# Optimization experiments

Hardware: AMD Instinct MI355X
Metric: run time of the kernel (lower is better)

The kernel has to match this reference:

```python
import jax, jax.numpy as jnp
import numpy as np

C = 512
EPS = 1e-5


def _layer_norm(x, gamma, beta):
    mu = jnp.mean(x, axis=-1, keepdims=True)
    var = jnp.var(x, axis=-1, keepdims=True)
    return (x - mu) * jax.lax.rsqrt(var + EPS) * gamma + beta


def setup_inputs() -> dict:
    key = jax.random.key(0)
    ks = jax.random.split(key, 12)
    B, L = 8, 2048
    s = 1.0 / np.sqrt(C)
    return {
        "x1": jax.random.normal(ks[0], (B, C, L), dtype=jnp.float32),
        "x2": jax.random.normal(ks[1], (B, C, L), dtype=jnp.float32),
        "w_q": jax.random.normal(ks[2], (C, C), dtype=jnp.float32) * s,
        "b_q": jax.random.normal(ks[3], (C,), dtype=jnp.float32) * s,
        "w_k": jax.random.normal(ks[4], (C, C), dtype=jnp.float32) * s,
        "b_k": jax.random.normal(ks[5], (C,), dtype=jnp.float32) * s,
        "w_v1": jax.random.normal(ks[6], (C, C), dtype=jnp.float32) * s,
        "b_v1": jax.random.normal(ks[7], (C,), dtype=jnp.float32) * s,
        "w_v2": jax.random.normal(ks[8], (C, C), dtype=jnp.float32) * s,
        "b_v2": jax.random.normal(ks[9], (C,), dtype=jnp.float32) * s,
        "ln_gamma": jnp.ones((C,), dtype=jnp.float32),
        "ln_beta": jnp.zeros((C,), dtype=jnp.float32),
    }


def reference(x1, x2, w_q, b_q, w_k, b_k, w_v1, b_v1, w_v2, b_v2, ln_gamma, ln_beta):
    # (B, C, L) -> (B, L, C)
    x1 = jnp.swapaxes(x1, 1, 2)
    x2 = jnp.swapaxes(x2, 1, 2)
    # torch Linear: y = x @ W^T + b
    q = jnp.einsum("blc,dc->bld", x1, w_q) + b_q
    k = jnp.einsum("blc,dc->bld", x2, w_k) + b_k
    v1 = jnp.einsum("blc,dc->bld", x1, w_v1) + b_v1
    v2 = jnp.einsum("blc,dc->bld", x2, w_v2) + b_v2
    # shared attention scores [B, L1, L2]
    attn = jnp.einsum("bqc,bkc->bqk", q, k) / jnp.sqrt(jnp.float32(C))
    attn_k = jax.nn.softmax(attn, axis=-1)          # rows (over L2)
    attn_q = jax.nn.softmax(attn, axis=1)           # cols (over L1)
    vk = jnp.einsum("bqk,bkc->bqc", attn_k, v2)     # [B, L1, C]
    vq = jnp.einsum("bqk,bqc->bkc", attn_q, v1)     # [B, L2, C]
    # cross skip + shared layernorm
    r1 = _layer_norm(vk + x1, ln_gamma, ln_beta)
    r2 = _layer_norm(vq + x2, ln_gamma, ln_beta)
    return (jnp.swapaxes(r1, 1, 2), jnp.swapaxes(r2, 1, 2))
```

## Files before the change

kernel.cpp:

```cpp
#include <hip/hip_runtime.h>

#define L_DIM 2048
#define C_DIM 512
#define B_DIM 8

typedef __attribute__((ext_vector_type(8))) short bf16x8;
typedef __attribute__((ext_vector_type(4))) float f32x4;

constexpr size_t SQ  = (size_t)L_DIM * C_DIM;
constexpr size_t SAT = (size_t)L_DIM * L_DIM;
constexpr size_t MC  = (size_t)B_DIM * L_DIM * C_DIM;
constexpr int BL = B_DIM * L_DIM;

__device__ float g_psr[16][BL];
__device__ float g_psc[16][BL];

__device__ __forceinline__ float bf2f(ushort u) {
  union { float f; unsigned int i; } c; c.i = ((unsigned int)u) << 16; return c.f;
}
__device__ __forceinline__ ushort f2bf(float f) {
  union { float f; unsigned int i; } c; c.f = f;
  unsigned int lsb = (c.i >> 16) & 1u;
  return (ushort)((c.i + 0x7FFFu + lsb) >> 16);
}

__device__ __forceinline__ float wave_red_sum(float v) {
  #pragma unroll
  for (int o = 1; o < 64; o <<= 1) v += __shfl_xor(v, o, 64);
  return v;
}

__device__ __forceinline__ void glds16(const ushort* g, ushort* l) {
  __builtin_amdgcn_global_load_lds(
      (const __attribute__((address_space(1))) void*)g,
      (__attribute__((address_space(3))) void*)l, 16, 0, 0);
}

__device__ __forceinline__ int slotAB(int r, int c) {
  return (((c ^ (r & 7)) + (r >> 3)) & 7);
}
__device__ __forceinline__ int chAB(int r, int sl) {
  return ((sl - (r >> 3)) & 7) ^ (r & 7);
}
__device__ __forceinline__ int slotC(int r, int q4) {
  return ((q4 ^ (r & 15)) + (r >> 4)) & 15;
}

__device__ __forceinline__ int xcd_swz(int bid, int nwg) {
  return (bid & 7) * (nwg >> 3) + (bid >> 3);
}

template <bool STATS, bool SCALE>
__device__ __forceinline__ void gemm_core128(
    const ushort* __restrict__ Ab, const ushort* __restrict__ Bb,
    const float* __restrict__ bias,
    ushort* __restrict__ obN, ushort* __restrict__ obT,
    const int K, const int lda, const int ldb, const int ldo, const int ldoT,
    const int m0, const int n0, const float scale, const int EPI,
    const int sb, const float* __restrict__ ps)
{
  __shared__ __align__(16) ushort lds[16384];
  __shared__ float sinv[128];

  const int t = threadIdx.x;
  const int lane = t & 63, w = t >> 6;
  const int wr = w >> 1, wc = w & 1;
  const int l16 = lane & 15, lhi = lane >> 4;
  const int lrow = lane >> 3, lsl = lane & 7;

  ushort* As = lds;
  ushort* Bs = lds + 8192;

  if (SCALE) {
    if (t < 128) {
      float s = 0.f;
      #pragma unroll
      for (int p = 0; p < 16; ++p) s += ps[(size_t)p * BL + t];
      sinv[t] = 1.0f / s;
    }
  }

  f32x4 acc[4][4];
  #pragma unroll
  for (int i = 0; i < 4; ++i)
    #pragma unroll
    for (int j = 0; j < 4; ++j) { f32x4 zv = {0.f, 0.f, 0.f, 0.f}; acc[i][j] = zv; }

  const int KT = K >> 6;
  for (int kt = 0; kt < KT; ++kt) {
    const int k0 = kt << 6;
    __syncthreads();
    #pragma unroll
    for (int p = 0; p < 4; ++p) {
      const int rbase = w * 32 + p * 8;
      const int rr = rbase + lrow;
      const int ch = chAB(rr, lsl);
      glds16(Ab + (size_t)(m0 + rr) * lda + k0 + ch * 8, As + rbase * 64);
      glds16(Bb + (size_t)(n0 + rr) * ldb + k0 + ch * 8, Bs + rbase * 64);
    }
    __syncthreads();
    #pragma unroll
    for (int ks = 0; ks < 2; ++ks) {
      bf16x8 af[4], bg[4];
      #pragma unroll
      for (int i = 0; i < 4; ++i) {
        const int ra = wr * 64 + i * 16 + l16;
        af[i] = *(const bf16x8*)&As[ra * 64 + 8 * slotAB(ra, ks * 4 + lhi)];
        const int rb = wc * 64 + i * 16 + l16;
        bg[i] = *(const bf16x8*)&Bs[rb * 64 + 8 * slotAB(rb, ks * 4 + lhi)];
      }
      #pragma unroll
      for (int i = 0; i < 4; ++i)
        #pragma unroll
        for (int j = 0; j < 4; ++j)
          acc[i][j] = __builtin_amdgcn_mfma_f32_16x16x32_bf16(af[i], bg[j], acc[i][j], 0, 0, 0);
    }
  }

  __syncthreads();
  ushort* Cs = lds;
  #pragma unroll
  for (int i = 0; i < 4; ++i) {
    #pragma unroll
    for (int j = 0; j < 4; ++j) {
      const int er = wr * 64 + i * 16 + lhi * 4;
      const int ec = wc * 64 + j * 16 + l16;
      const float bv = bias ? bias[n0 + ec] : 0.f;
      #pragma unroll
      for (int r = 0; r < 4; ++r) {
        const int rr = er + r;
        float val = acc[i][j][r] * scale + bv;
        if (STATS) val = __expf(val);
        if (SCALE) val *= sinv[rr];
        Cs[rr * 128 + 8 * slotC(rr, ec >> 3) + (ec & 7)] = f2bf(val);
      }
    }
  }
  __syncthreads();
  if (EPI == 0 || EPI == 2) {
    #pragma unroll
    for (int p = 0; p < 8; ++p) {
      const int id = p * 256 + t, r = id >> 4, cc = id & 15;
      const bf16x8 v = *(const bf16x8*)&Cs[r * 128 + 8 * slotC(r, cc)];
      *(bf16x8*)(obN + (size_t)(m0 + r) * ldo + n0 + cc * 8) = v;
    }
  }
  if (EPI >= 1) {
    #pragma unroll
    for (int p = 0; p < 8; ++p) {
      const int id = p * 256 + t, c = id >> 4, rs = id & 15;
      bf16x8 tv;
      #pragma unroll
      for (int jj = 0; jj < 8; ++jj) {
        const int r2 = rs * 8 + jj;
        tv[jj] = (short)Cs[r2 * 128 + 8 * slotC(r2, c >> 3) + (c & 7)];
      }
      *(bf16x8*)(obT + (size_t)(n0 + c) * ldoT + m0 + rs * 8) = tv;
    }
  }

  if (STATS) {
    if (t < 128) {
      const int r = t;
      float s = 0.f;
      #pragma unroll
      for (int cc = 0; cc < 16; ++cc) {
        const bf16x8 v8 = *(const bf16x8*)&Cs[r * 128 + 8 * slotC(r, cc)];
        #pragma unroll
        for (int j = 0; j < 8; ++j) s += bf2f((ushort)v8[j]);
      }
      g_psr[n0 >> 7][sb * L_DIM + m0 + r] = s;
    } else {
      const int c = t - 128;
      float s = 0.f;
      #pragma unroll 8
      for (int r2 = 0; r2 < 128; ++r2)
        s += bf2f(Cs[r2 * 128 + 8 * slotC(r2, c >> 3) + (c & 7)]);
      g_psc[m0 >> 7][sb * L_DIM + n0 + c] = s;
    }
  }
}

__global__ __launch_bounds__(256, 4) void gemm_proj(
    const ushort* __restrict__ x1T, const ushort* __restrict__ x2T,
    const ushort* __restrict__ wbf,
    const float* __restrict__ b_q, const float* __restrict__ b_k,
    const float* __restrict__ b_v1, const float* __restrict__ b_v2,
    ushort* __restrict__ q, ushort* __restrict__ kb,
    ushort* __restrict__ v1T, ushort* __restrict__ v2T)
{
  const int lid = xcd_swz(blockIdx.x, 2048);
  const int x = lid & 15, y = (lid >> 4) & 3, rest = lid >> 6;
  const int b = rest & 7, pj = rest >> 3;
  const ushort* A = ((pj & 1) ? x2T : x1T) + (size_t)b * SQ;
  const ushort* B = wbf + (size_t)pj * (C_DIM * C_DIM);
  const float* bias = pj == 0 ? b_q : pj == 1 ? b_k : pj == 2 ? b_v1 : b_v2;
  if (pj < 2) {
    ushort* oN = (pj == 0 ? q : kb) + (size_t)b * SQ;
    gemm_core128<false, false>(A, B, bias, oN, nullptr, C_DIM, C_DIM, C_DIM,
                               C_DIM, 0, x * 128, y * 128, 1.0f, 0, 0, nullptr);
  } else {
    ushort* oT = (pj == 2 ? v1T : v2T) + (size_t)b * SQ;
    gemm_core128<false, false>(A, B, bias, nullptr, oT, C_DIM, C_DIM, C_DIM,
                               0, L_DIM, x * 128, y * 128, 1.0f, 1, 0, nullptr);
  }
}

__global__ __launch_bounds__(256, 4) void gemm_qkt(
    const ushort* __restrict__ qb, const ushort* __restrict__ kb,
    ushort* __restrict__ attn, ushort* __restrict__ attnT, const float scale)
{
  const int lid = xcd_swz(blockIdx.x, 2048);
  const int x = lid & 15, y = (lid >> 4) & 15, b = lid >> 8;
  gemm_core128<true, false>(qb + (size_t)b * SQ, kb + (size_t)b * SQ, nullptr,
               attn + (size_t)b * SAT, attnT + (size_t)b * SAT,
               C_DIM, C_DIM, C_DIM, L_DIM, L_DIM,
               x * 128, y * 128, scale, 2, b, nullptr);
}

__global__ __launch_bounds__(256, 4) void gemm_pv(
    const ushort* __restrict__ attn, const ushort* __restrict__ attnT,
    const ushort* __restrict__ v1T, const ushort* __restrict__ v2T,
    ushort* __restrict__ vk, ushort* __restrict__ vq)
{
  const int lid = xcd_swz(blockIdx.x, 1024);
  const int x = lid & 15, y = (lid >> 4) & 3, rest = lid >> 6;
  const int which = rest & 1, b = rest >> 1;
  const ushort* A = (which ? attnT : attn) + (size_t)b * SAT;
  const ushort* B = (which ? v1T : v2T) + (size_t)b * SQ;
  ushort* o = (which ? vq : vk) + (size_t)b * SQ;
  const int m0 = x * 128;
  const float* ps = (which ? &g_psc[0][0] : &g_psr[0][0]) + b * L_DIM + m0;
  gemm_core128<false, true>(A, B, nullptr, o, nullptr,
               L_DIM, L_DIM, L_DIM, C_DIM, 0,
               m0, y * 128, 1.0f, 0, b, ps);
}

__global__ __launch_bounds__(256) void xpose(const float* __restrict__ x1,
                                             const float* __restrict__ x2,
                                             ushort* __restrict__ xT)
{
  __shared__ float s[64][65];
  const int z = blockIdx.z, l0 = blockIdx.x * 64, c0 = blockIdx.y * 64;
  const int t = threadIdx.x;
  const float* xb = (z < 8 ? x1 : x2) + ((size_t)(z & 7) * C_DIM + c0) * L_DIM + l0;
  #pragma unroll
  for (int p = 0; p < 16; ++p) {
    const int c = p * 4 + (t >> 6);
    s[c][t & 63] = xb[(size_t)c * L_DIM + (t & 63)];
  }
  __syncthreads();
  ushort* ob = xT + (size_t)z * SQ + (size_t)l0 * C_DIM + c0;
  #pragma unroll
  for (int p = 0; p < 16; ++p) {
    const int l = p * 4 + (t >> 6);
    ob[(size_t)l * C_DIM + (t & 63)] = f2bf(s[t & 63][l]);
  }
}

__global__ __launch_bounds__(256) void cvtw4(const float* __restrict__ a,
    const float* __restrict__ b, const float* __restrict__ c,
    const float* __restrict__ d, ushort* __restrict__ o)
{
  const int i = blockIdx.x * 256 + threadIdx.x;
  const int sel = i >> 18;
  const float* w = sel == 0 ? a : sel == 1 ? b : sel == 2 ? c : d;
  o[i] = f2bf(w[i & 262143]);
}

__global__ __launch_bounds__(256) void ln_out(const ushort* __restrict__ vk,
    const ushort* __restrict__ vq, const float* __restrict__ x1,
    const float* __restrict__ x2, const float* __restrict__ gamma,
    const float* __restrict__ beta, float* __restrict__ out)
{
  __shared__ __align__(16) ushort s[32][520];
  __shared__ float mu[32], rsd[32];
  __shared__ float gb[512], bb[512];
  const int t = threadIdx.x;
  const int b = blockIdx.y, l0 = blockIdx.x * 32, which = blockIdx.z;
  const ushort* vx = which ? vq : vk;
  const float* xo = which ? x2 : x1;
  float* obase = out + (size_t)which * MC;
  #pragma unroll
  for (int r = 0; r < 2; ++r) { gb[r * 256 + t] = gamma[r * 256 + t]; bb[r * 256 + t] = beta[r * 256 + t]; }
  const ushort* vb = vx + ((size_t)b * L_DIM + l0) * C_DIM;
  #pragma unroll
  for (int p = 0; p < 8; ++p) {
    const int id = p * 256 + t;
    const int l = id >> 6, cb = (id & 63) * 8;
    *(bf16x8*)&s[l][cb] = *(const bf16x8*)&vb[(size_t)l * C_DIM + cb];
  }
  __syncthreads();
  const float* xb = xo + (size_t)b * C_DIM * L_DIM + l0;
  for (int it = 0; it < 64; ++it) {
    const int idx = it * 256 + t, c = idx >> 5, l = idx & 31;
    s[l][c] = f2bf(bf2f(s[l][c]) + xb[(size_t)c * L_DIM + l]);
  }
  __syncthreads();
  const int w = t >> 6, lane = t & 63;
  #pragma unroll
  for (int rr = 0; rr < 8; ++rr) {
    const int l = w * 8 + rr;
    const bf16x8 v8 = *(const bf16x8*)&s[l][lane * 8];
    float sum = 0.f, sq = 0.f;
    #pragma unroll
    for (int j = 0; j < 8; ++j) {
      const float v = bf2f((ushort)v8[j]);
      sum += v; sq = fmaf(v, v, sq);
    }
    sum = wave_red_sum(sum); sq = wave_red_sum(sq);
    if (lane == 0) {
      const float m = sum * (1.f / 512.f);
      const float var = sq * (1.f / 512.f) - m * m;
      mu[l] = m; rsd[l] = rsqrtf(var + 1e-5f);
    }
  }
  __syncthreads();
  float* ob = obase + (size_t)b * C_DIM * L_DIM + l0;
  for (int it = 0; it < 64; ++it) {
    const int idx = it * 256 + t, c = idx >> 5, l = idx & 31;
    const float v = (bf2f(s[l][c]) - mu[l]) * rsd[l] * gb[c] + bb[c];
    ob[(size_t)c * L_DIM + l] = v;
  }
}

extern "C" void kernel_launch(void* const* d_in, const int* in_sizes, int n_in,
                              void* d_out, int out_size, void* d_ws, size_t ws_size,
                              hipStream_t stream) {
  const float* x1   = (const float*)d_in[0];
  const float* x2   = (const float*)d_in[1];
  const float* w_q  = (const float*)d_in[2];
  const float* b_q  = (const float*)d_in[3];
  const float* w_k  = (const float*)d_in[4];
  const float* b_k  = (const float*)d_in[5];
  const float* w_v1 = (const float*)d_in[6];
  const float* b_v1 = (const float*)d_in[7];
  const float* w_v2 = (const float*)d_in[8];
  const float* b_v2 = (const float*)d_in[9];
  const float* gamma= (const float*)d_in[10];
  const float* beta = (const float*)d_in[11];
  float* out = (float*)d_out;

  ushort* q    = (ushort*)d_ws;
  ushort* kbuf = q + MC;
  ushort* v1T  = kbuf + MC;
  ushort* v2T  = v1T + MC;
  ushort* attn = v2T + MC;
  ushort* x1T = attn;
  ushort* wbf = attn + 2 * MC;
  ushort* vkbuf = kbuf;
  ushort* vqbuf = q;
  ushort* attnT = (ushort*)d_out;

  const float iscale = 0.044194173824159216f;
  const dim3 blk256(256);

  cvtw4<<<4096, blk256, 0, stream>>>(w_q, w_k, w_v1, w_v2, wbf);
  xpose<<<dim3(32, 8, 16), blk256, 0, stream>>>(x1, x2, x1T);
  gemm_proj<<<2048, blk256, 0, stream>>>(x1T, x1T + MC, wbf,
      b_q, b_k, b_v1, b_v2, q, kbuf, v1T, v2T);
  gemm_qkt<<<2048, blk256, 0, stream>>>(q, kbuf, attn, attnT, iscale);
  gemm_pv<<<1024, blk256, 0, stream>>>(attn, attnT, v1T, v2T, vkbuf, vqbuf);
  ln_out<<<dim3(L_DIM / 32, B_DIM, 2), blk256, 0, stream>>>(
      vkbuf, vqbuf, x1, x2, gamma, beta, out);
}
```

Baseline: 239.7 us.

## Triple-buffer GEMM LDS tiles with BK=32 and async prefetch two stages ahead

Restructures the shared GEMM core from a single-buffered BK=64 loop with two __syncthreads per iteration into a three-stage ring of BK=32 LDS tiles. Global-to-LDS loads run two k-steps ahead, with explicit vmcnt waits and one barrier per iteration, and the LDS swizzle is changed to match 32-wide rows. The aim is to hide global load latency behind the MFMA work. In exchange, LDS use grows and occupancy hints drop from 4 to 3 blocks per CU. The hand-counted waitcnts must also stay correct.

```diff
diff --git a/kernel.cpp b/kernel.cpp
--- a/kernel.cpp
+++ b/kernel.cpp
@@ -36,11 +36,11 @@
       (__attribute__((address_space(3))) void*)l, 16, 0, 0);
 }
 
-__device__ __forceinline__ int slotAB(int r, int c) {
-  return (((c ^ (r & 7)) + (r >> 3)) & 7);
-}
-__device__ __forceinline__ int chAB(int r, int sl) {
-  return ((sl - (r >> 3)) & 7) ^ (r & 7);
+__device__ __forceinline__ int slot32(int r, int c) {
+  return (((c ^ (r & 3)) + (r >> 2)) & 3);
+}
+__device__ __forceinline__ int ch32(int r, int sl) {
+  return (((sl - (r >> 2)) & 3) ^ (r & 3));
 }
 __device__ __forceinline__ int slotC(int r, int q4) {
   return ((q4 ^ (r & 15)) + (r >> 4)) & 15;
@@ -59,17 +59,14 @@
     const int m0, const int n0, const float scale, const int EPI,
     const int sb, const float* __restrict__ ps)
 {
-  __shared__ __align__(16) ushort lds[16384];
+  __shared__ __align__(16) ushort lds[24576];
   __shared__ float sinv[128];
 
   const int t = threadIdx.x;
   const int lane = t & 63, w = t >> 6;
   const int wr = w >> 1, wc = w & 1;
   const int l16 = lane & 15, lhi = lane >> 4;
-  const int lrow = lane >> 3, lsl = lane & 7;
-
-  ushort* As = lds;
-  ushort* Bs = lds + 8192;
+  const int lrow4 = lane >> 2, lsl4 = lane & 3;
 
   if (SCALE) {
     if (t < 128) {
@@ -86,38 +83,59 @@
     #pragma unroll
     for (int j = 0; j < 4; ++j) { f32x4 zv = {0.f, 0.f, 0.f, 0.f}; acc[i][j] = zv; }
 
-  const int KT = K >> 6;
+  auto stage = [&](ushort* base, int k0) {
+    #pragma unroll
+    for (int p = 0; p < 2; ++p) {
+      const int rbase = w * 32 + p * 16;
+      const int rr = rbase + lrow4;
+      const int ch = ch32(rr, lsl4);
+      glds16(Ab + (size_t)(m0 + rr) * lda + k0 + ch * 8, base + rbase * 32);
+    }
+    #pragma unroll
+    for (int p = 0; p < 2; ++p) {
+      const int rbase = w * 32 + p * 16;
+      const int rr = rbase + lrow4;
+      const int ch = ch32(rr, lsl4);
+      glds16(Bb + (size_t)(n0 + rr) * ldb + k0 + ch * 8, base + 4096 + rbase * 32);
+    }
+  };
+
+  const int KT = K >> 5;
+  ushort* cur = lds;
+  ushort* nxt = lds + 8192;
+  ushort* fut = lds + 16384;
+  stage(cur, 0);
+  stage(nxt, 32);
+  __builtin_amdgcn_sched_barrier(0);
+  asm volatile("s_waitcnt vmcnt(4) lgkmcnt(0)" ::: "memory");
+  __builtin_amdgcn_s_barrier();
+  __builtin_amdgcn_sched_barrier(0);
+
   for (int kt = 0; kt < KT; ++kt) {
-    const int k0 = kt << 6;
-    __syncthreads();
-    #pragma unroll
-    for (int p = 0; p < 4; ++p) {
-      const int rbase = w * 32 + p * 8;
-      const int rr = rbase + lrow;
-      const int ch = chAB(rr, lsl);
-      glds16(Ab + (size_t)(m0 + rr) * lda + k0 + ch * 8, As + rbase * 64);
-      glds16(Bb + (size_t)(n0 + rr) * ldb + k0 + ch * 8, Bs + rbase * 64);
-    }
-    __syncthreads();
-    #pragma unroll
-    for (int ks = 0; ks < 2; ++ks) {
-      bf16x8 af[4], bg[4];
-      #pragma unroll
-      for (int i = 0; i < 4; ++i) {
-        const int ra = wr * 64 + i * 16 + l16;
-        af[i] = *(const bf16x8*)&As[ra * 64 + 8 * slotAB(ra, ks * 4 + lhi)];
-        const int rb = wc * 64 + i * 16 + l16;
-        bg[i] = *(const bf16x8*)&Bs[rb * 64 + 8 * slotAB(rb, ks * 4 + lhi)];
-      }
-      #pragma unroll
-      for (int i = 0; i < 4; ++i)
-        #pragma unroll
-        for (int j = 0; j < 4; ++j)
-          acc[i][j] = __builtin_amdgcn_mfma_f32_16x16x32_bf16(af[i], bg[j], acc[i][j], 0, 0, 0);
-    }
-  }
-
-  __syncthreads();
+    if (kt + 2 < KT) stage(fut, (kt + 2) << 5);
+    const ushort* As = cur;
+    const ushort* Bs = cur + 4096;
+    bf16x8 af[4], bg[4];
+    #pragma unroll
+    for (int i = 0; i < 4; ++i) {
+      const int ra = wr * 64 + i * 16 + l16;
+      af[i] = *(const bf16x8*)&As[ra * 32 + 8 * slot32(ra, lhi)];
+      const int rb = wc * 64 + i * 16 + l16;
+      bg[i] = *(const bf16x8*)&Bs[rb * 32 + 8 * slot32(rb, lhi)];
+    }
+    #pragma unroll
+    for (int i = 0; i < 4; ++i)
+      #pragma unroll
+      for (int j = 0; j < 4; ++j)
+        acc[i][j] = __builtin_amdgcn_mfma_f32_16x16x32_bf16(af[i], bg[j], acc[i][j], 0, 0, 0);
+    __builtin_amdgcn_sched_barrier(0);
+    if (kt + 2 < KT)      asm volatile("s_waitcnt vmcnt(4)" ::: "memory");
+    else if (kt + 1 < KT) asm volatile("s_waitcnt vmcnt(0)" ::: "memory");
+    __builtin_amdgcn_s_barrier();
+    __builtin_amdgcn_sched_barrier(0);
+    ushort* tmp = cur; cur = nxt; nxt = fut; fut = tmp;
+  }
+
   ushort* Cs = lds;
   #pragma unroll
   for (int i = 0; i < 4; ++i) {
@@ -181,7 +199,7 @@
   }
 }
 
-__global__ __launch_bounds__(256, 4) void gemm_proj(
+__global__ __launch_bounds__(256, 3) void gemm_proj(
     const ushort* __restrict__ x1T, const ushort* __restrict__ x2T,
     const ushort* __restrict__ wbf,
     const float* __restrict__ b_q, const float* __restrict__ b_k,
@@ -206,7 +224,7 @@
   }
 }
 
-__global__ __launch_bounds__(256, 4) void gemm_qkt(
+__global__ __launch_bounds__(256, 3) void gemm_qkt(
     const ushort* __restrict__ qb, const ushort* __restrict__ kb,
     ushort* __restrict__ attn, ushort* __restrict__ attnT, const float scale)
 {
@@ -218,7 +236,7 @@
                x * 128, y * 128, scale, 2, b, nullptr);
 }
 
-__global__ __launch_bounds__(256, 4) void gemm_pv(
+__global__ __launch_bounds__(256, 3) void gemm_pv(
     const ushort* __restrict__ attn, const ushort* __restrict__ attnT,
     const ushort* __restrict__ v1T, const ushort* __restrict__ v2T,
     ushort* __restrict__ vk, ushort* __restrict__ vq)
```

After: 270.3 us. 12.8% more time.
